# Kernel tuning notes

Measured on AMD Instinct MI355X. Metric: run time of the kernel, lower is better.

Reference implementation:

```python
import jax, jax.numpy as jnp
import numpy as np


def _binarize_act(z):
    # STE: forward = sign(z), backward = d/dz clamp(z,-1,1)
    clipped = jnp.clip(z, -1.0, 1.0)
    return jax.lax.stop_gradient(jnp.sign(z) - clipped) + clipped


def _binarize_weight(w):
    # per-output-channel scaling factor = mean |w| over (in, kh, kw), detached
    scale = jax.lax.stop_gradient(jnp.mean(jnp.abs(w), axis=(1, 2, 3), keepdims=True))
    clipped = jnp.clip(w, -1.0, 1.0)
    return jax.lax.stop_gradient(scale * jnp.sign(w) - clipped) + clipped


def setup_inputs() -> dict:
    key = jax.random.key(0)
    k = jax.random.split(key, 6)
    B, C, H, W = 16, 64, 256, 256
    return {
        "x": jax.random.normal(k[0], (B, C, H, W), dtype=jnp.float32),
        "move0_bias": jax.random.normal(k[1], (1, C, 1, 1), dtype=jnp.float32) * 0.1,
        "conv_weight": jax.random.normal(k[2], (C, C, 3, 3), dtype=jnp.float32) * 0.1,
        "prelu_weight": jnp.full((C,), 0.25, dtype=jnp.float32)
        + jax.random.normal(k[3], (C,), dtype=jnp.float32) * 0.01,
        "pr_bias0": jax.random.normal(k[4], (1, C, 1, 1), dtype=jnp.float32) * 0.1,
        "pr_bias1": jax.random.normal(k[5], (1, C, 1, 1), dtype=jnp.float32) * 0.1,
    }


def reference(x, move0_bias, conv_weight, prelu_weight, pr_bias0, pr_bias1):
    identity = x  # stride=1, out_channels == in_channels -> no downsample / concat
    z = _binarize_act(x + move0_bias)
    bw = _binarize_weight(conv_weight)
    y = jax.lax.conv_general_dilated(
        z, bw, window_strides=(1, 1), padding=((1, 1), (1, 1)),
        dimension_numbers=("NCHW", "OIHW", "NCHW"))
    # RPReLU: bias0 -> per-channel PReLU -> bias1
    y = y + pr_bias0
    a = prelu_weight.reshape(1, -1, 1, 1)
    y = jnp.where(y > 0, y, a * y)
    y = y + pr_bias1
    return y + identity
```

## Files before the change

### kernel.cpp

```cpp
#include <hip/hip_runtime.h>
#include <stdint.h>

#define Bn 16
#define C 64
#define H 256
#define W 256
#define HW (H * W)
#define NHW (Bn * HW)

#define TW 64
#define TH 16
#define SZH 18
#define SZW 73

typedef float f32x4 __attribute__((ext_vector_type(4)));
typedef float f32x2 __attribute__((ext_vector_type(2)));

__global__ void prep_weights(const float* __restrict__ w,
                             const float* __restrict__ pb0,
                             const float* __restrict__ aw,
                             const float* __restrict__ pb1,
                             uint64_t* __restrict__ wbitsP,
                             float4* __restrict__ prm,
                             int2* __restrict__ edg) {
    int o = blockIdx.x;
    int c = threadIdx.x;
    const float* wp = w + ((size_t)o * C + c) * 9;
    float asum = 0.f;
    uint64_t m[9];
#pragma unroll
    for (int tap = 0; tap < 9; ++tap) {
        float v = wp[tap];
        asum += fabsf(v);
        m[tap] = __ballot(v > 0.f);
    }
    if (c == 0) {
#pragma unroll
        for (int tap = 0; tap < 9; ++tap) wbitsP[o * 10 + tap] = m[tap];
        wbitsP[o * 10 + 9] = 0;
        edg[o] = make_int2(
            2 * (int)(__popcll(m[0]) + __popcll(m[3]) + __popcll(m[6])) - 192,
            2 * (int)(__popcll(m[2]) + __popcll(m[5]) + __popcll(m[8])) - 192);
    }
#pragma unroll
    for (int off = 32; off > 0; off >>= 1)
        asum += __shfl_down(asum, off);
    if (c == 0) prm[o] = make_float4(asum * (1.f / 576.f), pb0[o], aw[o], pb1[o]);
}

__global__ __launch_bounds__(512, 2) void bconv_fused(
        const uint64_t* __restrict__ wbitsP,
        const float4* __restrict__ prm,
        const int2* __restrict__ edg,
        const float* __restrict__ x,
        const float* __restrict__ bias,
        float* __restrict__ out) {
    __shared__ uint64_t sz[SZH * SZW];

    int t = threadIdx.x;
    int bid = blockIdx.x;
    int n = bid >> 6;
    int tile = bid & 63;
    int ty = tile >> 2, tx = tile & 3;
    int gh0 = ty * TH, gw0 = tx * TW;

    const float* xn = x + (size_t)n * C * HW;

    if (t < SZH * 18) {
        int r = t / 18;
        int cb = (t - r * 18) * 4;
        int gh = gh0 + r - 1;
        int gwb = gw0 - 4 + cb;
        uint64_t b0 = 0, b1 = 0, b2 = 0, b3 = 0;
        if ((unsigned)gh < (unsigned)H && (unsigned)gwb <= (unsigned)(W - 4)) {
            const float* xp = xn + gh * W + gwb;
            f32x4 cur[8], nxt[8];
#pragma unroll
            for (int k = 0; k < 8; ++k)
                cur[k] = *reinterpret_cast<const f32x4*>(xp + (size_t)k * HW);
            for (int b8 = 0; b8 < 8; ++b8) {
                if (b8 < 7) {
#pragma unroll
                    for (int k = 0; k < 8; ++k)
                        nxt[k] = *reinterpret_cast<const f32x4*>(
                            xp + (size_t)((b8 + 1) * 8 + k) * HW);
                }
#pragma unroll
                for (int k = 0; k < 8; ++k) {
                    int ch = b8 * 8 + k;
                    float bc = bias[ch];
                    f32x4 v = cur[k];
                    b0 |= (uint64_t)(v.x + bc > 0.f) << ch;
                    b1 |= (uint64_t)(v.y + bc > 0.f) << ch;
                    b2 |= (uint64_t)(v.z + bc > 0.f) << ch;
                    b3 |= (uint64_t)(v.w + bc > 0.f) << ch;
                }
                if (b8 < 7) {
#pragma unroll
                    for (int k = 0; k < 8; ++k) cur[k] = nxt[k];
                }
            }
        }
        uint64_t* zp = &sz[r * SZW + cb];
        zp[0] = b0; zp[1] = b1; zp[2] = b2; zp[3] = b3;
    }
    __syncthreads();

    int tr = t >> 5;
    int tc2 = (t & 31) * 2;
    int gh = gh0 + tr;
    int gw = gw0 + tc2;

    uint64_t zb[3][4];
#pragma unroll
    for (int i = 0; i < 3; ++i)
#pragma unroll
        for (int j = 0; j < 4; ++j)
            zb[i][j] = sz[(tr + i) * SZW + tc2 + 3 + j];

    const float* xid = xn + gh * W + gw;
    float* op = out + (size_t)n * C * HW + gh * W + gw;
    bool leftE  = (gw == 0);
    bool rightE = (gw == W - 2);

    bool slowW = (ty == 0 && tr < 2) || (ty == 15 && tr >= 14);

    auto proc = [&](int oc, f32x2 iv) {
        const uint64_t* wp = wbitsP + oc * 10;
        int s0 = 0, s1 = 0;
#pragma unroll
        for (int i = 0; i < 3; ++i)
#pragma unroll
            for (int jj = 0; jj < 3; ++jj) {
                uint64_t wt = wp[i * 3 + jj];
                s0 += (int)__popcll(wt ^ zb[i][jj]);
                s1 += (int)__popcll(wt ^ zb[i][jj + 1]);
            }
        int d0 = 576 - 2 * s0, d1 = 576 - 2 * s1;
        int2 e = edg[oc];
        if (leftE)  d0 += e.x;
        if (rightE) d1 += e.y;
        float4 pr = prm[oc];
        f32x2 r;
        float y;
        y = pr.x * (float)d0 + pr.y; y = y > 0.f ? y : pr.z * y; r.x = y + pr.w + iv.x;
        y = pr.x * (float)d1 + pr.y; y = y > 0.f ? y : pr.z * y; r.y = y + pr.w + iv.y;
        __builtin_nontemporal_store(r, reinterpret_cast<f32x2*>(op + (size_t)oc * HW));
    };

    if (!slowW) {
        f32x2 idv[8], nid[8];
#pragma unroll
        for (int k = 0; k < 8; ++k)
            idv[k] = *reinterpret_cast<const f32x2*>(xid + (size_t)k * HW);
        for (int g = 0; g < 8; ++g) {
            int ob = g * 8;
            if (g < 7) {
#pragma unroll
                for (int k = 0; k < 8; ++k)
                    nid[k] = *reinterpret_cast<const f32x2*>(
                        xid + (size_t)(ob + 8 + k) * HW);
            }
#pragma unroll
            for (int k = 0; k < 8; ++k) proc(ob + k, idv[k]);
            if (g < 7) {
#pragma unroll
                for (int k = 0; k < 8; ++k) idv[k] = nid[k];
            }
        }
    } else {
        int vrow[3], vcol[4];
#pragma unroll
        for (int i = 0; i < 3; ++i)
            vrow[i] = ((unsigned)(gh - 1 + i) < (unsigned)H) ? -1 : 0;
#pragma unroll
        for (int j = 0; j < 4; ++j)
            vcol[j] = ((unsigned)(gw - 1 + j) < (unsigned)W) ? -1 : 0;
        int nr  = (vrow[0] & 1) + (vrow[1] & 1) + (vrow[2] & 1);
        int nv0 = nr * ((vcol[0] & 1) + (vcol[1] & 1) + (vcol[2] & 1));
        int nv1 = nr * ((vcol[1] & 1) + (vcol[2] & 1) + (vcol[3] & 1));
#pragma unroll 2
        for (int o = 0; o < C; ++o) {
            const uint64_t* wp = wbitsP + o * 10;
            int s0 = 0, s1 = 0;
#pragma unroll
            for (int i = 0; i < 3; ++i)
#pragma unroll
                for (int jj = 0; jj < 3; ++jj) {
                    uint64_t wt = wp[i * 3 + jj];
                    s0 += (vrow[i] & vcol[jj])     & (int)__popcll(wt ^ zb[i][jj]);
                    s1 += (vrow[i] & vcol[jj + 1]) & (int)__popcll(wt ^ zb[i][jj + 1]);
                }
            float4 pr = prm[o];
            f32x2 idv = *reinterpret_cast<const f32x2*>(xid + (size_t)o * HW);
            f32x2 r;
            float y;
            y = pr.x * (float)(64 * nv0 - 2 * s0) + pr.y; y = y > 0.f ? y : pr.z * y; r.x = y + pr.w + idv.x;
            y = pr.x * (float)(64 * nv1 - 2 * s1) + pr.y; y = y > 0.f ? y : pr.z * y; r.y = y + pr.w + idv.y;
            __builtin_nontemporal_store(r, reinterpret_cast<f32x2*>(op + (size_t)o * HW));
        }
    }
}

extern "C" void kernel_launch(void* const* d_in, const int* in_sizes, int n_in,
                              void* d_out, int out_size, void* d_ws, size_t ws_size,
                              hipStream_t stream) {
    const float* x           = (const float*)d_in[0];
    const float* move0_bias  = (const float*)d_in[1];
    const float* conv_weight = (const float*)d_in[2];
    const float* prelu_w     = (const float*)d_in[3];
    const float* pr_bias0    = (const float*)d_in[4];
    const float* pr_bias1    = (const float*)d_in[5];
    float* out = (float*)d_out;

    uint8_t* ws = (uint8_t*)d_ws;
    uint64_t* wbitsP = (uint64_t*)ws;
    float4* prm      = (float4*)(ws + 5120);
    int2* edg        = (int2*)(ws + 6144);

    prep_weights<<<64, 64, 0, stream>>>(conv_weight, pr_bias0, prelu_w, pr_bias1,
                                        wbitsP, prm, edg);
    bconv_fused<<<Bn * (H / TH) * (W / TW), 512, 0, stream>>>(
        wbitsP, prm, edg, x, move0_bias, out);
}
```

Measured before the change: 516.3 us.

## Software-pipeline identity loads and popcount across channel groups; swizzle block order

The main path is restructured into a two-stage software pipeline. It computes popcount dot products for the next group of 8 channels, packed as 16-bit pairs, and issues that group's identity loads while the current group's epilogue and stores run, so more load latency is hidden behind compute. The block index is also remapped so that consecutive launched blocks come from different images. This adds register pressure under the 512-thread, 2-blocks-per-SM launch bounds and could cause spills.

```diff
diff --git a/kernel.cpp b/kernel.cpp
--- a/kernel.cpp
+++ b/kernel.cpp
@@ -58,7 +58,7 @@
     __shared__ uint64_t sz[SZH * SZW];
 
     int t = threadIdx.x;
-    int bid = blockIdx.x;
+    int bid = (blockIdx.x & 7) * 128 + (blockIdx.x >> 3);
     int n = bid >> 6;
     int tile = bid & 63;
     int ty = tile >> 2, tx = tile & 3;
@@ -125,49 +125,67 @@
 
     bool slowW = (ty == 0 && tr < 2) || (ty == 15 && tr >= 14);
 
-    auto proc = [&](int oc, f32x2 iv) {
-        const uint64_t* wp = wbitsP + oc * 10;
-        int s0 = 0, s1 = 0;
-#pragma unroll
-        for (int i = 0; i < 3; ++i)
-#pragma unroll
-            for (int jj = 0; jj < 3; ++jj) {
-                uint64_t wt = wp[i * 3 + jj];
-                s0 += (int)__popcll(wt ^ zb[i][jj]);
-                s1 += (int)__popcll(wt ^ zb[i][jj + 1]);
+    if (!slowW) {
+        uint32_t dA[8], dB[8];
+        f32x2 idA[8], idB[8];
+
+        auto POPC = [&](uint32_t (&dst)[8], int gbase) {
+#pragma unroll
+            for (int k = 0; k < 8; ++k) {
+                int oc = gbase + k;
+                const uint64_t* wp = wbitsP + oc * 10;
+                int s0 = 0, s1 = 0;
+#pragma unroll
+                for (int i = 0; i < 3; ++i)
+#pragma unroll
+                    for (int jj = 0; jj < 3; ++jj) {
+                        uint64_t wt = wp[i * 3 + jj];
+                        s0 += (int)__popcll(wt ^ zb[i][jj]);
+                        s1 += (int)__popcll(wt ^ zb[i][jj + 1]);
+                    }
+                int d0 = 576 - 2 * s0, d1 = 576 - 2 * s1;
+                int2 e = edg[oc];
+                if (leftE)  d0 += e.x;
+                if (rightE) d1 += e.y;
+                dst[k] = (uint32_t)(d0 & 0xffff) | ((uint32_t)(d1 & 0xffff) << 16);
             }
-        int d0 = 576 - 2 * s0, d1 = 576 - 2 * s1;
-        int2 e = edg[oc];
-        if (leftE)  d0 += e.x;
-        if (rightE) d1 += e.y;
-        float4 pr = prm[oc];
-        f32x2 r;
-        float y;
-        y = pr.x * (float)d0 + pr.y; y = y > 0.f ? y : pr.z * y; r.x = y + pr.w + iv.x;
-        y = pr.x * (float)d1 + pr.y; y = y > 0.f ? y : pr.z * y; r.y = y + pr.w + iv.y;
-        __builtin_nontemporal_store(r, reinterpret_cast<f32x2*>(op + (size_t)oc * HW));
-    };
-
-    if (!slowW) {
-        f32x2 idv[8], nid[8];
-#pragma unroll
-        for (int k = 0; k < 8; ++k)
-            idv[k] = *reinterpret_cast<const f32x2*>(xid + (size_t)k * HW);
-        for (int g = 0; g < 8; ++g) {
-            int ob = g * 8;
-            if (g < 7) {
-#pragma unroll
-                for (int k = 0; k < 8; ++k)
-                    nid[k] = *reinterpret_cast<const f32x2*>(
-                        xid + (size_t)(ob + 8 + k) * HW);
+        };
+        auto LOADG = [&](f32x2 (&idst)[8], int gbase) {
+#pragma unroll
+            for (int k = 0; k < 8; ++k)
+                idst[k] = *reinterpret_cast<const f32x2*>(
+                    xid + (size_t)(gbase + k) * HW);
+        };
+        auto EPI = [&](const uint32_t (&dsrc)[8], const f32x2 (&isrc)[8],
+                       int gbase) {
+#pragma unroll
+            for (int k = 0; k < 8; ++k) {
+                int oc = gbase + k;
+                float4 pr = prm[oc];
+                int d0 = (int)(short)(dsrc[k] & 0xffff);
+                int d1 = (int)(short)(dsrc[k] >> 16);
+                f32x2 iv = isrc[k];
+                f32x2 r;
+                float y;
+                y = pr.x * (float)d0 + pr.y; y = y > 0.f ? y : pr.z * y;
+                r.x = y + pr.w + iv.x;
+                y = pr.x * (float)d1 + pr.y; y = y > 0.f ? y : pr.z * y;
+                r.y = y + pr.w + iv.y;
+                __builtin_nontemporal_store(
+                    r, reinterpret_cast<f32x2*>(op + (size_t)oc * HW));
             }
-#pragma unroll
-            for (int k = 0; k < 8; ++k) proc(ob + k, idv[k]);
-            if (g < 7) {
-#pragma unroll
-                for (int k = 0; k < 8; ++k) idv[k] = nid[k];
-            }
+        };
+
+        LOADG(idA, 0);  POPC(dA, 0);
+        LOADG(idB, 8);  POPC(dB, 8);
+        for (int g = 0; g < 48; g += 16) {
+            EPI(dA, idA, g);
+            LOADG(idA, g + 16);  POPC(dA, g + 16);
+            EPI(dB, idB, g + 8);
+            LOADG(idB, g + 24);  POPC(dB, g + 24);
         }
+        EPI(dA, idA, 48);
+        EPI(dB, idB, 56);
     } else {
         int vrow[3], vcol[4];
 #pragma unroll
```

Measured after the change: 560.8 us. 1.09x slower.
